# Performance work log

Hardware: AMD Instinct MI355X
Metric: run time of the kernel (lower is better)

The kernel has to match this reference:

```python
import jax, jax.numpy as jnp
import numpy as np

KS, ST, SS, TOP_N, WIN = 32, 16, 64, 16, 512  # kernel_size, stride, select_size, top_n, window_size
NEG = -1e30


def setup_inputs() -> dict:
    key = jax.random.key(0)
    k0, k1, k2, k3 = jax.random.split(key, 4)
    B, S, H, Dqk, Dv = 1, 2048, 16, 128, 128
    q = jax.random.normal(k0, (B, S, H, Dqk), jnp.float32)
    k = jax.random.normal(k1, (B, S, H, Dqk), jnp.float32)
    v = jax.random.normal(k2, (B, S, H, Dv), jnp.float32)
    w_gate = jax.random.normal(k3, (Dqk, 3), jnp.float32) * (Dqk ** -0.5)
    b_gate = jnp.zeros((3,), jnp.float32)
    return {"q": q, "k": k, "v": v, "w_gate": w_gate, "b_gate": b_gate}


def _masked_probs(scores, mask):
    # numerically safe masked softmax; rows with no valid key yield all-zero probs
    s = jnp.where(mask, scores, NEG)
    lse = jax.nn.logsumexp(s, axis=-1, keepdims=True)
    return jnp.where(mask, jnp.exp(s - lse), 0.0)


def _nsa_forward(q, k, v, w_gate, b_gate):
    B, S, H, Dqk = q.shape
    scale = Dqk ** -0.5
    C = (S - KS) // ST + 1          # number of compressed blocks
    NSEL = S // SS                  # number of selection blocks
    tpos = jnp.arange(S)

    # ---- branch 1: compressed attention (mean-pooled K/V blocks) ----
    wpos = jnp.arange(C)[:, None] * ST + jnp.arange(KS)[None, :]   # [C,KS]
    cmp_k = k[:, wpos].mean(axis=2)                                # [B,C,H,Dqk]
    cmp_v = v[:, wpos].mean(axis=2)                                # [B,C,H,Dv]
    s_cmp = jnp.einsum('bqhd,bchd->bhqc', q, cmp_k) * scale
    cmp_end = jnp.arange(C) * ST + KS - 1
    cmask = cmp_end[None, :] <= tpos[:, None]                      # block fully in past
    p_cmp = _masked_probs(s_cmp, cmask)                            # [B,H,S,C]
    cmp_o = jnp.einsum('bhqc,bchd->bqhd', p_cmp, cmp_v)

    # ---- top-n block selection from compressed attention probs ----
    c_start = jnp.arange(C) * ST
    j_start = jnp.arange(NSEL) * SS
    overlap = ((c_start[:, None] < j_start[None, :] + SS) &
               (c_start[:, None] + KS > j_start[None, :])).astype(q.dtype)  # [C,NSEL]
    p_sel = jnp.einsum('bhqc,cj->bhqj', p_cmp, overlap)            # [B,H,S,NSEL]
    allowed = j_start[None, :] <= tpos[:, None]                    # block started
    cur_oh = jax.nn.one_hot(tpos // SS, NSEL, dtype=q.dtype)       # force current block
    sc = jnp.where(allowed, p_sel, -1.0) + 1e6 * cur_oh
    _, idx = jax.lax.top_k(sc, TOP_N)                              # [B,H,S,TOP_N]

    # ---- shared dense scores (reference only; real kernel is IO-aware) ----
    s_full = jnp.einsum('bqhd,bkhd->bhqk', q, k) * scale           # [B,H,S,S]
    causal = tpos[None, :] <= tpos[:, None]

    # ---- branch 2: selected-block attention ----
    blk_mask = (idx[..., None] == jnp.arange(NSEL)).any(axis=-2)   # [B,H,S,NSEL]
    key_blk = tpos // SS
    sel_mask = blk_mask[..., key_blk] & causal                     # [B,H,S,S]
    p_s = _masked_probs(s_full, sel_mask)
    select_o = jnp.einsum('bhqk,bkhd->bqhd', p_s, v)

    # ---- branch 3: sliding-window causal attention ----
    wmask = causal & ((tpos[:, None] - tpos[None, :]) <= WIN)
    p_w = _masked_probs(s_full, wmask)
    window_o = jnp.einsum('bhqk,bkhd->bqhd', p_w, v)

    # ---- learned per-query gates ----
    gate = jax.nn.sigmoid(jnp.einsum('bqhd,dg->bqhg', q, w_gate) + b_gate)
    return (cmp_o * gate[..., 0:1] + select_o * gate[..., 1:2]
            + window_o * gate[..., 2:3])


def reference(q, k, v, w_gate, b_gate):
    return _nsa_forward(q, k, v, w_gate, b_gate)
```

## Files before the change

### kernel.cpp

```cpp
#include <hip/hip_runtime.h>

#define S_LEN 2048
#define NH 16
#define DIM 128
#define KSZ 32
#define STRD 16
#define SSZ 64
#define NSELB 32
#define NCMP 127
#define TOPN 16
#define WINSZ 512
#define NEGF (-1e30f)
#define NEGTH (-1e29f)
#define SCALE 0.088388347648318447f
#define SCALE2 (0.088388347648318447f * 1.4426950408889634f)

typedef __attribute__((ext_vector_type(8))) short bf16x8;
typedef __attribute__((ext_vector_type(4))) float f32x4;

__device__ __forceinline__ unsigned short f2bf(float f) {
  unsigned u = __builtin_bit_cast(unsigned, f);
  return (unsigned short)((u + 0x7FFFu + ((u >> 16) & 1u)) >> 16);
}
__device__ __forceinline__ float bf2f(unsigned short b) {
  return __builtin_bit_cast(float, (unsigned)b << 16);
}
__device__ __forceinline__ bf16x8 pack8(const float* f) {
  bf16x8 r;
#pragma unroll
  for (int i = 0; i < 8; ++i) r[i] = (short)f2bf(f[i]);
  return r;
}

#define SCIDX(r, c) ((r) * 132 + (((c) >> 5) * 33) + ((c) & 31))

__global__ __launch_bounds__(256) void nsa_build(
    const float* __restrict__ v, const float* __restrict__ k,
    unsigned short* __restrict__ vtg, unsigned short* __restrict__ kb) {
  const int c = blockIdx.x * 256 + threadIdx.x;
  {
    const int h = c >> 15, d = (c >> 8) & 127, tc = c & 255;
    float f[8];
#pragma unroll
    for (int i = 0; i < 8; ++i) f[i] = v[((tc * 8 + i) * NH + h) * DIM + d];
    *(bf16x8*)(vtg + ((h * DIM + d) * S_LEN + tc * 8)) = pack8(f);
  }
  {
    const int h = c >> 15, t = (c >> 4) & 2047, dc = c & 15;
    const float* src = k + ((t * NH + h) * DIM + dc * 8);
    float f[8];
#pragma unroll
    for (int i = 0; i < 8; ++i) f[i] = src[i];
    *(bf16x8*)(kb + ((h * S_LEN + t) * DIM + dc * 8)) = pack8(f);
  }
}

__global__ __launch_bounds__(128) void nsa_compress(
    const float* __restrict__ k, const float* __restrict__ v,
    unsigned short* __restrict__ cmpkh, unsigned short* __restrict__ cmpkl,
    unsigned short* __restrict__ cmpvt) {
  const int c = blockIdx.x & 127;
  const int h = blockIdx.x >> 7;
  const int d = threadIdx.x;
  float sk = 0.f, sv = 0.f;
  if (c < NCMP) {
    const int base = ((c * STRD) * NH + h) * DIM + d;
#pragma unroll
    for (int i = 0; i < KSZ; ++i) {
      sk += k[base + i * NH * DIM];
      sv += v[base + i * NH * DIM];
    }
    sk *= (1.0f / KSZ); sv *= (1.0f / KSZ);
  }
  const unsigned short hi = f2bf(sk);
  const unsigned short lo = f2bf(sk - bf2f(hi));
  cmpkh[(h * 128 + c) * 128 + d] = (c < NCMP) ? hi : 0;
  cmpkl[(h * 128 + c) * 128 + d] = (c < NCMP) ? lo : 0;
  cmpvt[(h * 128 + d) * 128 + c] = (c < NCMP) ? f2bf(sv) : 0;
}

__global__ __launch_bounds__(64, 2) void nsa_main(
    const float* __restrict__ q, const float* __restrict__ wg,
    const float* __restrict__ bg, const unsigned short* __restrict__ kb,
    const unsigned short* __restrict__ vtg,
    const unsigned short* __restrict__ cmpkh, const unsigned short* __restrict__ cmpkl,
    const unsigned short* __restrict__ cmpvt, float* __restrict__ out) {
  __shared__ float scw[16 * 132];
  __shared__ __align__(16) char pa[2112];
  __shared__ float gatesLds[48];
  __shared__ unsigned maskLds[16];

  const int b = blockIdx.x;
  const int h = ((b & 7) << 1) | ((b >> 3) & 1);
  const int tq0 = (127 - (b >> 4)) << 4;
  const int lane = threadIdx.x;
  const int l15 = lane & 15;
  const int l4 = lane >> 4;

  const int nvmax = tq0 >> 4;
  const int nct0 = (nvmax + 31) >> 5;
  const int nct = (nct0 < 4) ? nct0 : 4;

  if (lane < 16) maskLds[lane] = 0u;

  const unsigned short* kbh = kb + h * S_LEN * DIM;
  const unsigned short* vth = vtg + h * DIM * S_LEN;

  bf16x8 qfh[4];
  const float* qp = q + ((tq0 + l15) * NH + h) * DIM + l4 * 8;
#pragma unroll
  for (int ks = 0; ks < 4; ++ks) {
    float f[8];
#pragma unroll
    for (int i = 0; i < 8; ++i) f[i] = bf2f(f2bf(qp[ks * 32 + i]));
    qfh[ks] = pack8(f);
  }

  if (lane < 48) {
    const int qloc = lane / 3, gi = lane % 3;
    const float* qr_ = q + ((tq0 + qloc) * NH + h) * DIM;
    float acc = bg[gi];
#pragma unroll
    for (int d4 = 0; d4 < DIM; d4 += 4) {
      const float4 qv = *(const float4*)(qr_ + d4);
      acc += qv.x * wg[(d4 + 0) * 3 + gi] + qv.y * wg[(d4 + 1) * 3 + gi] +
             qv.z * wg[(d4 + 2) * 3 + gi] + qv.w * wg[(d4 + 3) * 3 + gi];
    }
    gatesLds[qloc * 3 + gi] = 1.0f / (1.0f + __expf(-acc));
  }

  {
    bf16x8 qfl[4];
#pragma unroll
    for (int ks = 0; ks < 4; ++ks) {
      float f[8];
#pragma unroll
      for (int i = 0; i < 8; ++i) {
        const float x = qp[ks * 32 + i];
        f[i] = x - bf2f(f2bf(x));
      }
      qfl[ks] = pack8(f);
    }
    for (int ct = 0; ct < nct; ++ct) {
      const unsigned short* bk = cmpkh + (h * 128 + ct * 32) * 128 + l4 * 8;
      const unsigned short* bkl = cmpkl + (h * 128 + ct * 32) * 128 + l4 * 8;
      f32x4 s0 = {0, 0, 0, 0}, s1 = {0, 0, 0, 0};
#pragma unroll
      for (int ks = 0; ks < 4; ++ks) {
        bf16x8 bh0 = *(const bf16x8*)(bk + l15 * 128 + ks * 32);
        bf16x8 bh1 = *(const bf16x8*)(bk + (16 + l15) * 128 + ks * 32);
        bf16x8 bl0 = *(const bf16x8*)(bkl + l15 * 128 + ks * 32);
        bf16x8 bl1 = *(const bf16x8*)(bkl + (16 + l15) * 128 + ks * 32);
        s0 = __builtin_amdgcn_mfma_f32_16x16x32_bf16(qfh[ks], bh0, s0, 0, 0, 0);
        s0 = __builtin_amdgcn_mfma_f32_16x16x32_bf16(qfl[ks], bh0, s0, 0, 0, 0);
        s0 = __builtin_amdgcn_mfma_f32_16x16x32_bf16(qfh[ks], bl0, s0, 0, 0, 0);
        s1 = __builtin_amdgcn_mfma_f32_16x16x32_bf16(qfh[ks], bh1, s1, 0, 0, 0);
        s1 = __builtin_amdgcn_mfma_f32_16x16x32_bf16(qfl[ks], bh1, s1, 0, 0, 0);
        s1 = __builtin_amdgcn_mfma_f32_16x16x32_bf16(qfh[ks], bl1, s1, 0, 0, 0);
      }
#pragma unroll
      for (int j = 0; j < 4; ++j) {
        const int qr = l4 * 4 + j;
        scw[SCIDX(qr, ct * 32 + l15)] = s0[j] * SCALE;
        scw[SCIDX(qr, ct * 32 + 16 + l15)] = s1[j] * SCALE;
      }
    }
  }

  {
    const int qq = lane >> 2, qg = lane & 3;
    const int tq = tq0 + qq;
    const int nv = (tq >= KSZ - 1) ? ((tq - (KSZ - 1)) / STRD + 1) : 0;
    float x[32];
#pragma unroll
    for (int i = 0; i < 32; ++i) x[i] = scw[SCIDX(qq, qg * 32 + i)];
    float m = NEGF;
#pragma unroll
    for (int i = 0; i < 32; ++i)
      if (qg * 32 + i < nv) m = fmaxf(m, x[i]);
    m = fmaxf(m, __shfl_xor(m, 1));
    m = fmaxf(m, __shfl_xor(m, 2));
    float s = 0.f;
#pragma unroll
    for (int i = 0; i < 32; ++i) {
      x[i] = (qg * 32 + i < nv) ? __expf(x[i] - m) : 0.f;
      s += x[i];
    }
    s += __shfl_xor(s, 1);
    s += __shfl_xor(s, 2);
    const float inv = (nv > 0) ? (1.0f / s) : 0.f;
#pragma unroll
    for (int i = 0; i < 32; ++i) scw[SCIDX(qq, qg * 32 + i)] = x[i] * inv;
  }

  {
    float* ssel = (float*)pa;
    const int qq = lane >> 2, jg = lane & 3;
    const int tq = tq0 + qq;
    float vj[8];
#pragma unroll
    for (int i = 0; i < 8; ++i) {
      const int j = jg * 8 + i;
      const int lo = (4 * j - 1 > 0) ? 4 * j - 1 : 0;
      const int hi = (4 * j + 3 < NCMP - 1) ? 4 * j + 3 : NCMP - 1;
      float ps = 0.f;
      for (int c = lo; c <= hi; ++c) ps += scw[SCIDX(qq, c)];
      float val = (j * SSZ <= tq) ? ps : -1.0f;
      if (j == (tq >> 6)) val += 1e6f;
      vj[i] = val;
      ssel[qq * 33 + j] = val;
    }
    float sv[32];
#pragma unroll
    for (int jp = 0; jp < 32; ++jp) sv[jp] = ssel[qq * 33 + jp];
#pragma unroll
    for (int i = 0; i < 8; ++i) {
      const int j = jg * 8 + i;
      const float my = vj[i];
      int rank = 0;
#pragma unroll
      for (int jp = 0; jp < 32; ++jp)
        rank += (sv[jp] > my) || (sv[jp] == my && jp < j);
      if (rank < TOPN && (j * SSZ <= tq)) atomicOr(&maskLds[qq], 1u << j);
    }
  }

  unsigned maskq[4];
#pragma unroll
  for (int j = 0; j < 4; ++j) maskq[j] = maskLds[l4 * 4 + j];
  unsigned sel16 = maskq[0] | maskq[1] | maskq[2] | maskq[3];
  sel16 |= __shfl_xor(sel16, 16);
  sel16 |= __shfl_xor(sel16, 32);

  {
    f32x4 accC[8];
#pragma unroll
    for (int n = 0; n < 8; ++n) accC[n] = (f32x4){0, 0, 0, 0};
    for (int ct = 0; ct < nct; ++ct) {
      float f[8];
#pragma unroll
      for (int i = 0; i < 8; ++i) f[i] = scw[SCIDX(l15, ct * 32 + l4 * 8 + i)];
      bf16x8 ap = pack8(f);
      const unsigned short* cvb = cmpvt + (h * 128) * 128 + ct * 32 + l4 * 8;
#pragma unroll
      for (int n = 0; n < 8; ++n) {
        bf16x8 bvv = *(const bf16x8*)(cvb + (n * 16 + l15) * 128);
        accC[n] = __builtin_amdgcn_mfma_f32_16x16x32_bf16(ap, bvv, accC[n], 0, 0, 0);
      }
    }
#pragma unroll
    for (int j = 0; j < 4; ++j) {
      const int qr = l4 * 4 + j;
      const float g0 = gatesLds[qr * 3 + 0];
#pragma unroll
      for (int n = 0; n < 8; ++n) scw[SCIDX(qr, n * 16 + l15)] = g0 * accC[n][j];
    }
  }

  const int ktmax = (tq0 + 15) >> 5;
  const int ktw = (tq0 > WINSZ) ? ((tq0 - WINSZ) >> 5) : 0;
  unsigned long long actmask;
  {
    unsigned long long m = (unsigned long long)sel16;
    m = (m | (m << 16)) & 0x0000FFFF0000FFFFull;
    m = (m | (m << 8))  & 0x00FF00FF00FF00FFull;
    m = (m | (m << 4))  & 0x0F0F0F0F0F0F0F0Full;
    m = (m | (m << 2))  & 0x3333333333333333ull;
    m = (m | (m << 1))  & 0x5555555555555555ull;
    const unsigned long long em = m * 3ull;
    const unsigned long long winm = ~0ull << ktw;
    const unsigned long long rng =
        (ktmax >= 63) ? ~0ull : ((1ull << (ktmax + 1)) - 1ull);
    actmask = (em | winm) & rng;
  }

  f32x4 accS[8], accW[8];
#pragma unroll
  for (int n = 0; n < 8; ++n) { accS[n] = (f32x4){0, 0, 0, 0}; accW[n] = (f32x4){0, 0, 0, 0}; }
  float mS[4], lS[4], mW[4], lW[4];
#pragma unroll
  for (int j = 0; j < 4; ++j) { mS[j] = NEGF; lS[j] = 0.f; mW[j] = NEGF; lW[j] = 0.f; }

  char* paS = pa;
  char* paW = pa + 1024;

  unsigned long long rem = actmask;
  int kt = rem ? __builtin_ctzll(rem) : 0;
  bf16x8 kf[8];
  if (rem) {
    const unsigned short* kbase = kbh + (kt << 5) * DIM + l4 * 8;
#pragma unroll
    for (int ks = 0; ks < 4; ++ks) {
      kf[ks] = *(const bf16x8*)(kbase + l15 * DIM + ks * 32);
      kf[4 + ks] = *(const bf16x8*)(kbase + (16 + l15) * DIM + ks * 32);
    }
  }

  while (rem) {
    rem &= rem - 1ull;
    const int kt0 = kt << 5;
    const int jb = kt >> 1;
    const bool selAct = (sel16 >> jb) & 1u;
    const bool winAct = kt >= ktw;
    const int ktn = rem ? __builtin_ctzll(rem) : -1;

    __builtin_amdgcn_s_setprio(1);
    f32x4 s0 = {0, 0, 0, 0}, s1 = {0, 0, 0, 0};
#pragma unroll
    for (int ks = 0; ks < 4; ++ks) {
      s0 = __builtin_amdgcn_mfma_f32_16x16x32_bf16(qfh[ks], kf[ks], s0, 0, 0, 0);
      s1 = __builtin_amdgcn_mfma_f32_16x16x32_bf16(qfh[ks], kf[4 + ks], s1, 0, 0, 0);
    }
    __builtin_amdgcn_s_setprio(0);

    bf16x8 bv[8];
    const unsigned short* vbase = vth + kt0 + l4 * 8;
#pragma unroll
    for (int n = 0; n < 8; ++n)
      bv[n] = *(const bf16x8*)(vbase + (n * 16 + l15) * S_LEN);

    if (ktn >= 0) {
      const unsigned short* kbase = kbh + (ktn << 5) * DIM + l4 * 8;
#pragma unroll
      for (int ks = 0; ks < 4; ++ks) {
        kf[ks] = *(const bf16x8*)(kbase + l15 * DIM + ks * 32);
        kf[4 + ks] = *(const bf16x8*)(kbase + (16 + l15) * DIM + ks * 32);
      }
    }

    const int c0 = kt0 + l15, c1 = kt0 + 16 + l15;
#pragma unroll
    for (int j = 0; j < 4; ++j) {
      const int qr = l4 * 4 + j;
      const int tq = tq0 + qr;
      const float sv0 = s0[j] * SCALE2, sv1 = s1[j] * SCALE2;
      if (selAct) {
        const bool mb = (maskq[j] >> jb) & 1u;
        const float v0 = (mb && c0 <= tq) ? sv0 : NEGF;
        const float v1 = (mb && c1 <= tq) ? sv1 : NEGF;
        const float rml = fmaxf(v0, v1);
        if (__any(rml > mS[j] + 11.5416541f)) {
          float rm = rml;
          rm = fmaxf(rm, __shfl_xor(rm, 1));
          rm = fmaxf(rm, __shfl_xor(rm, 2));
          rm = fmaxf(rm, __shfl_xor(rm, 4));
          rm = fmaxf(rm, __shfl_xor(rm, 8));
          if (rm > mS[j]) {
            const float sf = exp2f(mS[j] - rm);
            lS[j] *= sf;
#pragma unroll
            for (int n = 0; n < 8; ++n) accS[n][j] *= sf;
            mS[j] = rm;
          }
        }
        const float p0 = (v0 > NEGTH) ? exp2f(v0 - mS[j]) : 0.f;
        const float p1 = (v1 > NEGTH) ? exp2f(v1 - mS[j]) : 0.f;
        lS[j] += p0 + p1;
        *(unsigned short*)(paS + qr * 64 + ((l15 * 2) ^ (j << 4))) = f2bf(p0);
        *(unsigned short*)(paS + qr * 64 + (((16 + l15) * 2) ^ (j << 4))) = f2bf(p1);
      }
      if (winAct) {
        const float v0 = (c0 <= tq && c0 >= tq - WINSZ) ? sv0 : NEGF;
        const float v1 = (c1 <= tq && c1 >= tq - WINSZ) ? sv1 : NEGF;
        const float rml = fmaxf(v0, v1);
        if (__any(rml > mW[j] + 11.5416541f)) {
          float rm = rml;
          rm = fmaxf(rm, __shfl_xor(rm, 1));
          rm = fmaxf(rm, __shfl_xor(rm, 2));
          rm = fmaxf(rm, __shfl_xor(rm, 4));
          rm = fmaxf(rm, __shfl_xor(rm, 8));
          if (rm > mW[j]) {
            const float sf = exp2f(mW[j] - rm);
            lW[j] *= sf;
#pragma unroll
            for (int n = 0; n < 8; ++n) accW[n][j] *= sf;
            mW[j] = rm;
          }
        }
        const float p0 = (v0 > NEGTH) ? exp2f(v0 - mW[j]) : 0.f;
        const float p1 = (v1 > NEGTH) ? exp2f(v1 - mW[j]) : 0.f;
        lW[j] += p0 + p1;
        *(unsigned short*)(paW + qr * 64 + ((l15 * 2) ^ (j << 4))) = f2bf(p0);
        *(unsigned short*)(paW + qr * 64 + (((16 + l15) * 2) ^ (j << 4))) = f2bf(p1);
      }
    }
    __builtin_amdgcn_s_setprio(1);
    if (selAct) {
      bf16x8 ap = *(const bf16x8*)(paS + l15 * 64 + ((l4 * 16) ^ ((l15 & 3) << 4)));
#pragma unroll
      for (int n = 0; n < 8; ++n)
        accS[n] = __builtin_amdgcn_mfma_f32_16x16x32_bf16(ap, bv[n], accS[n], 0, 0, 0);
    }
    if (winAct) {
      bf16x8 ap = *(const bf16x8*)(paW + l15 * 64 + ((l4 * 16) ^ ((l15 & 3) << 4)));
#pragma unroll
      for (int n = 0; n < 8; ++n)
        accW[n] = __builtin_amdgcn_mfma_f32_16x16x32_bf16(ap, bv[n], accW[n], 0, 0, 0);
    }
    __builtin_amdgcn_s_setprio(0);
    kt = ktn;
  }

#pragma unroll
  for (int j = 0; j < 4; ++j) {
    float ls = lS[j], lw = lW[j];
    ls += __shfl_xor(ls, 1); lw += __shfl_xor(lw, 1);
    ls += __shfl_xor(ls, 2); lw += __shfl_xor(lw, 2);
    ls += __shfl_xor(ls, 4); lw += __shfl_xor(lw, 4);
    ls += __shfl_xor(ls, 8); lw += __shfl_xor(lw, 8);
    const int qr = l4 * 4 + j;
    const int tq = tq0 + qr;
    const float rlS = gatesLds[qr * 3 + 1] / ls;
    const float rlW = gatesLds[qr * 3 + 2] / lw;
#pragma unroll
    for (int n = 0; n < 8; ++n)
      out[(tq * NH + h) * DIM + n * 16 + l15] =
          scw[SCIDX(qr, n * 16 + l15)] + accS[n][j] * rlS + accW[n][j] * rlW;
  }
}

extern "C" void kernel_launch(void* const* d_in, const int* in_sizes, int n_in,
                              void* d_out, int out_size, void* d_ws, size_t ws_size,
                              hipStream_t stream) {
  const float* q  = (const float*)d_in[0];
  const float* k  = (const float*)d_in[1];
  const float* v  = (const float*)d_in[2];
  const float* wg = (const float*)d_in[3];
  const float* bg = (const float*)d_in[4];
  float* out = (float*)d_out;

  unsigned short* vtg   = (unsigned short*)d_ws;
  unsigned short* kb    = vtg + NH * DIM * S_LEN;
  unsigned short* cmpkh = kb + NH * S_LEN * DIM;
  unsigned short* cmpkl = cmpkh + NH * 128 * 128;
  unsigned short* cmpvt = cmpkl + NH * 128 * 128;

  nsa_build<<<2048, 256, 0, stream>>>(v, k, vtg, kb);
  nsa_compress<<<NH * 128, 128, 0, stream>>>(k, v, cmpkh, cmpkl, cmpvt);
  nsa_main<<<2048, 64, 0, stream>>>(q, wg, bg, kb, vtg, cmpkh, cmpkl, cmpvt, out);
}
```

Measured before the change: 229.3 us.

## Split key tiles across two waves per block with flash-style softmax merge

The main kernel moves from one wave to two waves per block. The active key tiles are dealt out alternately to each wave, and the compressed-score tiles and the gate and compressed-output work are also divided between the waves. Per-wave online-softmax partial sums for the selected and window branches are merged through LDS, using published max and sum values before the final write. This aims to cut per-block latency on the long key loop, at the cost of extra syncs, LDS use and a serial merge phase. Launch bounds change to 128 threads with 3 blocks per CU.

Result: slower. 358.6 us (+56.4%).

```diff
diff --git a/kernel.cpp b/kernel.cpp
--- a/kernel.cpp
+++ b/kernel.cpp
@@ -14,6 +14,7 @@
 #define NEGTH (-1e29f)
 #define SCALE 0.088388347648318447f
 #define SCALE2 (0.088388347648318447f * 1.4426950408889634f)
+#define DEFER2 11.5415603f
 
 typedef __attribute__((ext_vector_type(8))) short bf16x8;
 typedef __attribute__((ext_vector_type(4))) float f32x4;
@@ -79,21 +80,25 @@
   cmpvt[(h * 128 + d) * 128 + c] = (c < NCMP) ? f2bf(sv) : 0;
 }
 
-__global__ __launch_bounds__(64, 2) void nsa_main(
+__global__ __launch_bounds__(128, 3) void nsa_main(
     const float* __restrict__ q, const float* __restrict__ wg,
     const float* __restrict__ bg, const unsigned short* __restrict__ kb,
     const unsigned short* __restrict__ vtg,
     const unsigned short* __restrict__ cmpkh, const unsigned short* __restrict__ cmpkl,
     const unsigned short* __restrict__ cmpvt, float* __restrict__ out) {
   __shared__ float scw[16 * 132];
-  __shared__ __align__(16) char pa[2112];
+  __shared__ __align__(16) char pa[4096];
+  __shared__ float mergeBuf[16 * 132];
   __shared__ float gatesLds[48];
   __shared__ unsigned maskLds[16];
+  __shared__ float mlPub[32];
 
   const int b = blockIdx.x;
   const int h = ((b & 7) << 1) | ((b >> 3) & 1);
   const int tq0 = (127 - (b >> 4)) << 4;
-  const int lane = threadIdx.x;
+  const int tid = threadIdx.x;
+  const int lane = tid & 63;
+  const int w = tid >> 6;
   const int l15 = lane & 15;
   const int l4 = lane >> 4;
 
@@ -101,8 +106,6 @@
   const int nct0 = (nvmax + 31) >> 5;
   const int nct = (nct0 < 4) ? nct0 : 4;
 
-  if (lane < 16) maskLds[lane] = 0u;
-
   const unsigned short* kbh = kb + h * S_LEN * DIM;
   const unsigned short* vth = vtg + h * DIM * S_LEN;
 
@@ -116,7 +119,8 @@
     qfh[ks] = pack8(f);
   }
 
-  if (lane < 48) {
+  if (w == 0 && lane < 16) maskLds[lane] = 0u;
+  if (w == 1 && lane < 48) {
     const int qloc = lane / 3, gi = lane % 3;
     const float* qr_ = q + ((tq0 + qloc) * NH + h) * DIM;
     float acc = bg[gi];
@@ -128,7 +132,6 @@
     }
     gatesLds[qloc * 3 + gi] = 1.0f / (1.0f + __expf(-acc));
   }
-
   {
     bf16x8 qfl[4];
 #pragma unroll
@@ -141,7 +144,11 @@
       }
       qfl[ks] = pack8(f);
     }
-    for (int ct = 0; ct < nct; ++ct) {
+    const int ctbase = w * 2;
+#pragma unroll
+    for (int cc = 0; cc < 2; ++cc) {
+      const int ct = ctbase + cc;
+      if (ct >= nct) continue;
       const unsigned short* bk = cmpkh + (h * 128 + ct * 32) * 128 + l4 * 8;
       const unsigned short* bkl = cmpkl + (h * 128 + ct * 32) * 128 + l4 * 8;
       f32x4 s0 = {0, 0, 0, 0}, s1 = {0, 0, 0, 0};
@@ -167,63 +174,68 @@
     }
   }
 
-  {
-    const int qq = lane >> 2, qg = lane & 3;
-    const int tq = tq0 + qq;
-    const int nv = (tq >= KSZ - 1) ? ((tq - (KSZ - 1)) / STRD + 1) : 0;
-    float x[32];
-#pragma unroll
-    for (int i = 0; i < 32; ++i) x[i] = scw[SCIDX(qq, qg * 32 + i)];
-    float m = NEGF;
-#pragma unroll
-    for (int i = 0; i < 32; ++i)
-      if (qg * 32 + i < nv) m = fmaxf(m, x[i]);
-    m = fmaxf(m, __shfl_xor(m, 1));
-    m = fmaxf(m, __shfl_xor(m, 2));
-    float s = 0.f;
-#pragma unroll
-    for (int i = 0; i < 32; ++i) {
-      x[i] = (qg * 32 + i < nv) ? __expf(x[i] - m) : 0.f;
-      s += x[i];
-    }
-    s += __shfl_xor(s, 1);
-    s += __shfl_xor(s, 2);
-    const float inv = (nv > 0) ? (1.0f / s) : 0.f;
-#pragma unroll
-    for (int i = 0; i < 32; ++i) scw[SCIDX(qq, qg * 32 + i)] = x[i] * inv;
-  }
-
-  {
-    float* ssel = (float*)pa;
-    const int qq = lane >> 2, jg = lane & 3;
-    const int tq = tq0 + qq;
-    float vj[8];
-#pragma unroll
-    for (int i = 0; i < 8; ++i) {
-      const int j = jg * 8 + i;
-      const int lo = (4 * j - 1 > 0) ? 4 * j - 1 : 0;
-      const int hi = (4 * j + 3 < NCMP - 1) ? 4 * j + 3 : NCMP - 1;
-      float ps = 0.f;
-      for (int c = lo; c <= hi; ++c) ps += scw[SCIDX(qq, c)];
-      float val = (j * SSZ <= tq) ? ps : -1.0f;
-      if (j == (tq >> 6)) val += 1e6f;
-      vj[i] = val;
-      ssel[qq * 33 + j] = val;
-    }
-    float sv[32];
-#pragma unroll
-    for (int jp = 0; jp < 32; ++jp) sv[jp] = ssel[qq * 33 + jp];
-#pragma unroll
-    for (int i = 0; i < 8; ++i) {
-      const int j = jg * 8 + i;
-      const float my = vj[i];
-      int rank = 0;
-#pragma unroll
-      for (int jp = 0; jp < 32; ++jp)
-        rank += (sv[jp] > my) || (sv[jp] == my && jp < j);
-      if (rank < TOPN && (j * SSZ <= tq)) atomicOr(&maskLds[qq], 1u << j);
-    }
-  }
+  __syncthreads();
+
+  if (w == 0) {
+    {
+      const int qq = lane >> 2, qg = lane & 3;
+      const int tq = tq0 + qq;
+      const int nv = (tq >= KSZ - 1) ? ((tq - (KSZ - 1)) / STRD + 1) : 0;
+      float x[32];
+#pragma unroll
+      for (int i = 0; i < 32; ++i) x[i] = scw[SCIDX(qq, qg * 32 + i)];
+      float m = NEGF;
+#pragma unroll
+      for (int i = 0; i < 32; ++i)
+        if (qg * 32 + i < nv) m = fmaxf(m, x[i]);
+      m = fmaxf(m, __shfl_xor(m, 1));
+      m = fmaxf(m, __shfl_xor(m, 2));
+      float s = 0.f;
+#pragma unroll
+      for (int i = 0; i < 32; ++i) {
+        x[i] = (qg * 32 + i < nv) ? __expf(x[i] - m) : 0.f;
+        s += x[i];
+      }
+      s += __shfl_xor(s, 1);
+      s += __shfl_xor(s, 2);
+      const float inv = (nv > 0) ? (1.0f / s) : 0.f;
+#pragma unroll
+      for (int i = 0; i < 32; ++i) scw[SCIDX(qq, qg * 32 + i)] = x[i] * inv;
+    }
+    {
+      float* ssel = (float*)pa;
+      const int qq = lane >> 2, jg = lane & 3;
+      const int tq = tq0 + qq;
+      float vj[8];
+#pragma unroll
+      for (int i = 0; i < 8; ++i) {
+        const int j = jg * 8 + i;
+        const int lo = (4 * j - 1 > 0) ? 4 * j - 1 : 0;
+        const int hi = (4 * j + 3 < NCMP - 1) ? 4 * j + 3 : NCMP - 1;
+        float ps = 0.f;
+        for (int c = lo; c <= hi; ++c) ps += scw[SCIDX(qq, c)];
+        float val = (j * SSZ <= tq) ? ps : -1.0f;
+        if (j == (tq >> 6)) val += 1e6f;
+        vj[i] = val;
+        ssel[qq * 33 + j] = val;
+      }
+      float sv[32];
+#pragma unroll
+      for (int jp = 0; jp < 32; ++jp) sv[jp] = ssel[qq * 33 + jp];
+#pragma unroll
+      for (int i = 0; i < 8; ++i) {
+        const int j = jg * 8 + i;
+        const float my = vj[i];
+        int rank = 0;
+#pragma unroll
+        for (int jp = 0; jp < 32; ++jp)
+          rank += (sv[jp] > my) || (sv[jp] == my && jp < j);
+        if (rank < TOPN && (j * SSZ <= tq)) atomicOr(&maskLds[qq], 1u << j);
+      }
+    }
+  }
+
+  __syncthreads();
 
   unsigned maskq[4];
 #pragma unroll
@@ -232,7 +244,7 @@
   sel16 |= __shfl_xor(sel16, 16);
   sel16 |= __shfl_xor(sel16, 32);
 
-  {
+  if (w == 1) {
     f32x4 accC[8];
 #pragma unroll
     for (int n = 0; n < 8; ++n) accC[n] = (f32x4){0, 0, 0, 0};
@@ -259,7 +271,7 @@
 
   const int ktmax = (tq0 + 15) >> 5;
   const int ktw = (tq0 > WINSZ) ? ((tq0 - WINSZ) >> 5) : 0;
-  unsigned long long actmask;
+  unsigned long long mymask;
   {
     unsigned long long m = (unsigned long long)sel16;
     m = (m | (m << 16)) & 0x0000FFFF0000FFFFull;
@@ -271,7 +283,15 @@
     const unsigned long long winm = ~0ull << ktw;
     const unsigned long long rng =
         (ktmax >= 63) ? ~0ull : ((1ull << (ktmax + 1)) - 1ull);
-    actmask = (em | winm) & rng;
+    unsigned long long act = (em | winm) & rng;
+    mymask = 0ull;
+    int i = 0;
+    while (act) {
+      const unsigned long long lb = act & (~act + 1ull);
+      if ((i & 1) == w) mymask |= lb;
+      act ^= lb;
+      ++i;
+    }
   }
 
   f32x4 accS[8], accW[8];
@@ -281,10 +301,10 @@
 #pragma unroll
   for (int j = 0; j < 4; ++j) { mS[j] = NEGF; lS[j] = 0.f; mW[j] = NEGF; lW[j] = 0.f; }
 
-  char* paS = pa;
-  char* paW = pa + 1024;
-
-  unsigned long long rem = actmask;
+  char* paS = pa + w * 2048;
+  char* paW = paS + 1024;
+
+  unsigned long long rem = mymask;
   int kt = rem ? __builtin_ctzll(rem) : 0;
   bf16x8 kf[8];
   if (rem) {
@@ -339,7 +359,7 @@
         const float v0 = (mb && c0 <= tq) ? sv0 : NEGF;
         const float v1 = (mb && c1 <= tq) ? sv1 : NEGF;
         const float rml = fmaxf(v0, v1);
-        if (__any(rml > mS[j] + 11.5416541f)) {
+        if (__any(rml > mS[j] + DEFER2)) {
           float rm = rml;
           rm = fmaxf(rm, __shfl_xor(rm, 1));
           rm = fmaxf(rm, __shfl_xor(rm, 2));
@@ -363,7 +383,7 @@
         const float v0 = (c0 <= tq && c0 >= tq - WINSZ) ? sv0 : NEGF;
         const float v1 = (c1 <= tq && c1 >= tq - WINSZ) ? sv1 : NEGF;
         const float rml = fmaxf(v0, v1);
-        if (__any(rml > mW[j] + 11.5416541f)) {
+        if (__any(rml > mW[j] + DEFER2)) {
           float rm = rml;
           rm = fmaxf(rm, __shfl_xor(rm, 1));
           rm = fmaxf(rm, __shfl_xor(rm, 2));
@@ -401,6 +421,7 @@
     kt = ktn;
   }
 
+  float lSr[4], lWr[4];
 #pragma unroll
   for (int j = 0; j < 4; ++j) {
     float ls = lS[j], lw = lW[j];
@@ -408,14 +429,64 @@
     ls += __shfl_xor(ls, 2); lw += __shfl_xor(lw, 2);
     ls += __shfl_xor(ls, 4); lw += __shfl_xor(lw, 4);
     ls += __shfl_xor(ls, 8); lw += __shfl_xor(lw, 8);
-    const int qr = l4 * 4 + j;
-    const int tq = tq0 + qr;
-    const float rlS = gatesLds[qr * 3 + 1] / ls;
-    const float rlW = gatesLds[qr * 3 + 2] / lw;
-#pragma unroll
-    for (int n = 0; n < 8; ++n)
-      out[(tq * NH + h) * DIM + n * 16 + l15] =
-          scw[SCIDX(qr, n * 16 + l15)] + accS[n][j] * rlS + accW[n][j] * rlW;
+    lSr[j] = ls; lWr[j] = lw;
+  }
+
+  if (w == 1) {
+#pragma unroll
+    for (int j = 0; j < 4; ++j) {
+      const int qr = l4 * 4 + j;
+      if (l15 == 0) { mlPub[qr * 2] = mS[j]; mlPub[qr * 2 + 1] = lSr[j]; }
+#pragma unroll
+      for (int n = 0; n < 8; ++n) mergeBuf[SCIDX(qr, n * 16 + l15)] = accS[n][j];
+    }
+  }
+  __syncthreads();
+  if (w == 0) {
+#pragma unroll
+    for (int j = 0; j < 4; ++j) {
+      const int qr = l4 * 4 + j;
+      const float m1 = mlPub[qr * 2], l1 = mlPub[qr * 2 + 1];
+      const float M = fmaxf(mS[j], m1);
+      const float e0 = (lSr[j] > 0.f) ? exp2f(mS[j] - M) : 0.f;
+      const float e1 = (l1 > 0.f) ? exp2f(m1 - M) : 0.f;
+      const float gi = gatesLds[qr * 3 + 1] / (lSr[j] * e0 + l1 * e1);
+      const float c0_ = gi * e0, c1_ = gi * e1;
+#pragma unroll
+      for (int n = 0; n < 8; ++n)
+        scw[SCIDX(qr, n * 16 + l15)] +=
+            accS[n][j] * c0_ + mergeBuf[SCIDX(qr, n * 16 + l15)] * c1_;
+    }
+  }
+  __syncthreads();
+
+  if (w == 1) {
+#pragma unroll
+    for (int j = 0; j < 4; ++j) {
+      const int qr = l4 * 4 + j;
+      if (l15 == 0) { mlPub[qr * 2] = mW[j]; mlPub[qr * 2 + 1] = lWr[j]; }
+#pragma unroll
+      for (int n = 0; n < 8; ++n) mergeBuf[SCIDX(qr, n * 16 + l15)] = accW[n][j];
+    }
+  }
+  __syncthreads();
+  if (w == 0) {
+#pragma unroll
+    for (int j = 0; j < 4; ++j) {
+      const int qr = l4 * 4 + j;
+      const int tq = tq0 + qr;
+      const float m1 = mlPub[qr * 2], l1 = mlPub[qr * 2 + 1];
+      const float M = fmaxf(mW[j], m1);
+      const float e0 = (lWr[j] > 0.f) ? exp2f(mW[j] - M) : 0.f;
+      const float e1 = (l1 > 0.f) ? exp2f(m1 - M) : 0.f;
+      const float gi = gatesLds[qr * 3 + 2] / (lWr[j] * e0 + l1 * e1);
+      const float c0_ = gi * e0, c1_ = gi * e1;
+#pragma unroll
+      for (int n = 0; n < 8; ++n)
+        out[(tq * NH + h) * DIM + n * 16 + l15] =
+            scw[SCIDX(qr, n * 16 + l15)] +
+            accW[n][j] * c0_ + mergeBuf[SCIDX(qr, n * 16 + l15)] * c1_;
+    }
   }
 }
 
@@ -437,5 +508,5 @@
 
   nsa_build<<<2048, 256, 0, stream>>>(v, k, vtg, kb);
   nsa_compress<<<NH * 128, 128, 0, stream>>>(k, v, cmpkh, cmpkl, cmpvt);
-  nsa_main<<<2048, 64, 0, stream>>>(q, wg, bg, kb, vtg, cmpkh, cmpkl, cmpvt, out);
-}
+  nsa_main<<<2048, 128, 0, stream>>>(q, wg, bg, kb, vtg, cmpkh, cmpkl, cmpvt, out);
+}
```
